# Optimization experiments

Hardware: AMD Instinct MI355X
Metric: run time of the kernel (lower is better)

The kernel has to match this reference:

```python
import jax, jax.numpy as jnp
import numpy as np

# Model dims (match torch defaults)
B, LF, FEAT = 2, 64, 80          # batch, local frames, mel features
H, SKIP, A = 64, 256, 256        # block hidden, skip_size, signal_channels
NL, CYC = 24, 6                  # num_layers, cycle_size
UP_K, UP_REP = 4, 75             # ConvTranspose kernel/stride, frame repeat
S = LF * UP_K * UP_REP           # signal length = 19200


def setup_inputs() -> dict:
    key = jax.random.key(0)
    ks = jax.random.split(key, 16)
    r = lambda i, sh: jax.random.normal(ks[i], sh, jnp.float32) * 0.1
    return {
        'local_features': jax.random.normal(ks[0], (B, LF, FEAT), jnp.float32),
        'gold_signal': jax.random.uniform(ks[1], (B, S), jnp.float32, minval=-1.0, maxval=1.0),
        'embed_w': r(2, (H,)), 'embed_b': r(3, (H,)),
        'tconv_w': r(4, (FEAT, FEAT, UP_K)), 'tconv_b': r(5, (FEAT,)),
        'cond_w': r(6, (NL * 2 * H, FEAT)), 'cond_b': r(7, (NL * 2 * H,)),
        'dilate_w': r(8, (NL, 2 * H, H, 2)), 'dilate_b': r(9, (NL, 2 * H)),
        'res_w': r(10, (NL - 1, H, H)), 'res_b': r(11, (NL - 1, H)),
        'skip_w': r(12, (NL, SKIP, H)), 'skip_b': r(13, (NL, SKIP)),
        'out1_w': r(14, (A, SKIP)), 'out2_w': r(15, (A, A)),
    }


def _causal_dilated(x, w, b, d):
    # x [B,C,T], w [O,C,2]; left-pad by d == torch padding=d then slicing off last d
    y = jax.lax.conv_general_dilated(x, w, window_strides=(1,), padding=[(d, 0)],
                                     rhs_dilation=(d,),
                                     dimension_numbers=('NCH', 'OIH', 'NCH'))
    return y + b[None, :, None]


def reference(local_features, gold_signal, embed_w, embed_b, tconv_w, tconv_b,
              cond_w, cond_b, dilate_w, dilate_b, res_w, res_b,
              skip_w, skip_b, out1_w, out2_w):
    # --- ConditionalFeaturesUpsample ---
    lf = jnp.transpose(local_features, (0, 2, 1))  # [B,FEAT,LF]
    # ConvTranspose1d(kernel=stride=UP_K): out[:, :, UP_K*i+k] = sum_c w[c,:,k]*x[:,c,i]
    up = jnp.einsum('bci,cok->boik', lf, tconv_w).reshape(B, FEAT, LF * UP_K)
    up = up + tconv_b[None, :, None]
    cond = jnp.einsum('oc,bct->bot', cond_w, up) + cond_b[None, :, None]  # [B, NL*2H, LF*4]
    cond = jnp.repeat(cond, UP_REP, axis=-1)                               # [B, NL*2H, S]
    cond = cond.reshape(B, NL, 2 * H, S)
    # --- embed (1x1 conv on 1-channel signal) ---
    x = gold_signal[:, None, :] * embed_w[None, :, None] + embed_b[None, :, None]  # [B,H,S]
    # --- residual stack ---
    skip_acc = jnp.zeros((B, SKIP, S), x.dtype)
    for i in range(NL):
        d = 2 ** (i % CYC)
        y = _causal_dilated(x, dilate_w[i], dilate_b[i], d) + cond[:, i]
        g = jnp.tanh(y[:, :H]) * jax.nn.sigmoid(y[:, H:])
        skip_acc = skip_acc + jnp.einsum('oc,bct->bot', skip_w[i], g) + skip_b[i][None, :, None]
        if i < NL - 1:
            x = jnp.einsum('oc,bct->bot', res_w[i], g) + res_b[i][None, :, None] + x
    # --- output head: ReLU -> 1x1 -> ReLU -> 1x1 -> LogSoftmax(channels) ---
    h = jax.nn.relu(skip_acc)
    h = jax.nn.relu(jnp.einsum('oc,bct->bot', out1_w, h))
    logits = jnp.einsum('oc,bct->bot', out2_w, h)
    return jax.nn.log_softmax(logits, axis=1)  # [B, A, S]
```

## Files before the change

### kernel.cpp

```cpp
#include <hip/hip_runtime.h>
#include <hip/hip_bf16.h>
#include <cstdint>
#include <cstddef>

namespace {

constexpr int kB = 2, kLF = 64, kFEAT = 80, kSKIP = 256, kA = 256;
constexpr int kNL = 24, kT4 = 256;
constexpr int kS = 19200;
constexpr int kGR = 64;
constexpr int kXR = kGR + kS;
constexpr int kK = kNL * 64;
constexpr int kNS = kB * kS;
constexpr int kP2 = 72;

typedef __attribute__((ext_vector_type(8))) short bf8_t;
typedef __attribute__((ext_vector_type(4))) float f4_t;

__device__ inline unsigned short f2bu(float f) {
  __hip_bfloat16 h = __float2bfloat16(f);
  return __builtin_bit_cast(unsigned short, h);
}
__device__ inline float b2f(unsigned short u) {
  unsigned x = (unsigned)u << 16;
  return __builtin_bit_cast(float, x);
}
__device__ inline float fast_gate(float a, float b) {
  a = fminf(fmaxf(a, -30.f), 30.f);
  b = fminf(fmaxf(b, -30.f), 30.f);
  const float ea = __expf(-2.f * a);
  const float eb = __expf(-b);
  return (1.f - ea) * __fdividef(1.f, (1.f + ea) * (1.f + eb));
}

__global__ void prep_kernel(const float* __restrict__ dw, const float* __restrict__ rw,
                            const float* __restrict__ sw, const float* __restrict__ w1,
                            const float* __restrict__ w2, unsigned short* __restrict__ wcb,
                            unsigned short* __restrict__ wrb, unsigned short* __restrict__ swb2,
                            unsigned short* __restrict__ w1f, unsigned short* __restrict__ w2f) {
  int idx = blockIdx.x * 256 + threadIdx.x;
  const int n0 = kNL * 2 * 128 * 64;
  const int n1 = (kNL - 1) * 64 * 64;
  const int n2 = 256 * kK;
  const int n3 = 65536;
  if (idx < n0) {
    int r = idx;
    const int l = r / 16384; r -= l * 16384;
    const int tap = r / 8192; r -= tap * 8192;
    const int o = r / 64; const int h = r - o * 64;
    wcb[idx] = f2bu(dw[((l * 128 + o) * 64 + h) * 2 + tap]);
    return;
  }
  idx -= n0;
  if (idx < n1) { wrb[idx] = f2bu(rw[idx]); return; }
  idx -= n1;
  if (idx < n2) {
    const int q = idx & 31;
    const int rest = idx >> 5;
    const int o = rest & 255;
    const int t = rest >> 8;
    const int kk = t & 1, kb = t >> 1;
    const int h = kk * 32 + q;
    swb2[idx] = f2bu(sw[((size_t)(kb * 256 + o)) * 64 + h]);
    return;
  }
  idx -= n2;
  if (idx < n3) {
    const int q = idx & 31;
    const int rest = idx >> 5;
    const int a = rest & 255, kk = rest >> 8;
    w1f[idx] = f2bu(w1[a * 256 + kk * 32 + q]);
    return;
  }
  idx -= n3;
  if (idx < n3) {
    const int q = idx & 31;
    const int rest = idx >> 5;
    const int a = rest & 255, kk = rest >> 8;
    w2f[idx] = f2bu(w2[a * 256 + kk * 32 + q]);
  }
}

__global__ void up_kernel(const float* __restrict__ lf, const float* __restrict__ tw,
                          const float* __restrict__ tb, float* __restrict__ up) {
  const int t40 = blockIdx.x * 16, b = blockIdx.y;
  __shared__ float lfS[4][80];
  const int tid = threadIdx.x;
  for (int idx = tid; idx < 320; idx += 256) {
    const int rr = idx / 80, cc = idx - rr * 80;
    lfS[rr][cc] = lf[((size_t)b * kLF + (t40 >> 2) + rr) * kFEAT + cc];
  }
  __syncthreads();
  const int t4l = tid & 15;
  const int cq = tid >> 4;
  const int ifr = t4l >> 2, kk = t4l & 3;
  for (int q = 0; q < 5; ++q) {
    const int c = cq * 5 + q;
    float s = tb[c];
    for (int cc = 0; cc < 80; ++cc) s += lfS[ifr][cc] * tw[(cc * 80 + c) * 4 + kk];
    up[((size_t)b * kFEAT + c) * 256 + t40 + t4l] = s;
  }
}

__global__ __launch_bounds__(256) void cond_gemm_kernel(
    const float* __restrict__ up, const float* __restrict__ cw,
    const float* __restrict__ cb, const float* __restrict__ dbf,
    float* __restrict__ cond) {
  const int o0 = blockIdx.x * 128, t40 = blockIdx.y * 64, b = blockIdx.z;
  __shared__ float upS[80][68];
  __shared__ float WS[128][84];
  const int tid = threadIdx.x;
  for (int r = 0; r < 5; ++r) {
    const int f4 = r * 256 + tid;
    const int row = f4 >> 4, c4 = (f4 & 15) << 2;
    *reinterpret_cast<float4*>(&upS[row][c4]) =
        *reinterpret_cast<const float4*>(up + ((size_t)b * kFEAT + row) * 256 + t40 + c4);
  }
  for (int r = 0; r < 10; ++r) {
    const int f4 = r * 256 + tid;
    const int row = f4 / 20, c4 = (f4 % 20) * 4;
    *reinterpret_cast<float4*>(&WS[row][c4]) =
        *reinterpret_cast<const float4*>(cw + (size_t)(o0 + row) * kFEAT + c4);
  }
  __syncthreads();
  const int tx = tid & 15, oy = tid >> 4;
  float4 acc[8];
#pragma unroll
  for (int j = 0; j < 8; ++j) acc[j] = make_float4(0.f, 0.f, 0.f, 0.f);
  for (int k0 = 0; k0 < 80; k0 += 4) {
    float4 b0 = *reinterpret_cast<const float4*>(&upS[k0 + 0][tx * 4]);
    float4 b1 = *reinterpret_cast<const float4*>(&upS[k0 + 1][tx * 4]);
    float4 b2 = *reinterpret_cast<const float4*>(&upS[k0 + 2][tx * 4]);
    float4 b3 = *reinterpret_cast<const float4*>(&upS[k0 + 3][tx * 4]);
#pragma unroll
    for (int j = 0; j < 8; ++j) {
      const float4 wj = *reinterpret_cast<const float4*>(&WS[oy * 8 + j][k0]);
      float4 a = acc[j];
      a.x += wj.x * b0.x + wj.y * b1.x + wj.z * b2.x + wj.w * b3.x;
      a.y += wj.x * b0.y + wj.y * b1.y + wj.z * b2.y + wj.w * b3.y;
      a.z += wj.x * b0.z + wj.y * b1.z + wj.z * b2.z + wj.w * b3.z;
      a.w += wj.x * b0.w + wj.y * b1.w + wj.z * b2.w + wj.w * b3.w;
      acc[j] = a;
    }
  }
  __syncthreads();
  float* ws2 = &WS[0][0];
#pragma unroll
  for (int j = 0; j < 8; ++j) {
    const int ol = oy * 8 + j;
    const int og = o0 + ol;
    const float bias = cb[og] + dbf[og];
    ws2[ol * 69 + tx * 4 + 0] = acc[j].x + bias;
    ws2[ol * 69 + tx * 4 + 1] = acc[j].y + bias;
    ws2[ol * 69 + tx * 4 + 2] = acc[j].z + bias;
    ws2[ol * 69 + tx * 4 + 3] = acc[j].w + bias;
  }
  __syncthreads();
  for (int r = 0; r < 8; ++r) {
    const int f = r * 256 + tid;
    const int row = f >> 5, c4 = (f & 31) << 2;
    float4 v;
    v.x = ws2[(c4 + 0) * 69 + row];
    v.y = ws2[(c4 + 1) * 69 + row];
    v.z = ws2[(c4 + 2) * 69 + row];
    v.w = ws2[(c4 + 3) * 69 + row];
    *reinterpret_cast<float4*>(cond + ((size_t)b * kT4 + t40 + row) * 3072 + o0 + c4) = v;
  }
}

__global__ void bias_sum_kernel(const float* __restrict__ sb, float* __restrict__ bs) {
  const int o = threadIdx.x;
  float s = 0.f;
  for (int i = 0; i < kNL; ++i) s += sb[i * kSKIP + o];
  bs[o] = s;
}

__global__ void embed_kernel(const float* __restrict__ sig, const float* __restrict__ ew,
                             const float* __restrict__ eb, unsigned short* __restrict__ xA,
                             unsigned short* __restrict__ xB) {
  const int idx = blockIdx.x * 256 + threadIdx.x;
  if (idx >= kB * kXR * 8) return;
  const int c8 = (idx & 7) << 3;
  const int row = (idx >> 3) % kXR;
  const int b = idx / (kXR * 8);
  const size_t off = ((size_t)b * kXR + row) * 64 + c8;
  if (row < kGR) {
    uint4 z = {0u, 0u, 0u, 0u};
    *reinterpret_cast<uint4*>(xA + off) = z;
    *reinterpret_cast<uint4*>(xB + off) = z;
  } else {
    const float s = sig[b * kS + row - kGR];
    unsigned short v[8];
#pragma unroll
    for (int q = 0; q < 8; ++q) v[q] = f2bu(s * ew[c8 + q] + eb[c8 + q]);
    *reinterpret_cast<uint4*>(xA + off) = *reinterpret_cast<uint4*>(v);
  }
}

__global__ __launch_bounds__(256) void layer_kernel(
    const unsigned short* __restrict__ x_in, unsigned short* __restrict__ x_out,
    const unsigned short* __restrict__ wcb,
    const unsigned short* __restrict__ wrb,
    const float* __restrict__ cond, const float* __restrict__ rb,
    unsigned short* __restrict__ gbuf, int layer, int d, int write_x) {
  const int b = blockIdx.y;
  const int t0 = blockIdx.x * 64;
  const int tid = threadIdx.x;
  const int lane = tid & 63, wv = tid >> 6;
  const int l15 = lane & 15, l4 = lane >> 4;
  const int nw = wv * 16;

  __shared__ alignas(16) unsigned short Wc[2][128][kP2];
  __shared__ alignas(16) unsigned short Wr[64][kP2];
  __shared__ alignas(16) unsigned short xww[96][kP2];
  __shared__ alignas(16) unsigned short gt[64][kP2];
  __shared__ alignas(16) unsigned short xo[64][kP2];
  __shared__ float cnd[2][128];
  __shared__ float rbs[64];

  const int c0 = t0 / 75;
  {
    const int ci = tid >> 7, o = tid & 127;
    int cc = c0 + ci; if (cc > 255) cc = 255;
    cnd[ci][o] = cond[((size_t)b * kT4 + cc) * 3072 + layer * 128 + o];
  }
  if (tid < 64) rbs[tid] = write_x ? rb[tid] : 0.f;
  for (int r = 0; r < 8; ++r) {
    const int f = r * 256 + tid;
    const int row = f >> 3, c8 = (f & 7) << 3;
    *reinterpret_cast<uint4*>(&Wc[row >> 7][row & 127][c8]) =
        *reinterpret_cast<const uint4*>(wcb + row * 64 + c8);
  }
  if (write_x) {
    for (int r = 0; r < 2; ++r) {
      const int f = r * 256 + tid;
      const int row = f >> 3, c8 = (f & 7) << 3;
      *reinterpret_cast<uint4*>(&Wr[row][c8]) =
          *reinterpret_cast<const uint4*>(wrb + row * 64 + c8);
    }
  }
  const unsigned short* xwin = x_in + ((size_t)b * kXR + kGR + t0 - 32) * 64;
  for (int r = 0; r < 3; ++r) {
    const int f = r * 256 + tid;
    const int row = f >> 3, c8 = (f & 7) << 3;
    *reinterpret_cast<uint4*>(&xww[row][c8]) =
        *reinterpret_cast<const uint4*>(xwin + (size_t)row * 64 + c8);
  }
  __syncthreads();

  f4_t acc[8];
#pragma unroll
  for (int i = 0; i < 8; ++i) acc[i] = (f4_t){0.f, 0.f, 0.f, 0.f};
#pragma unroll
  for (int kk = 0; kk < 2; ++kk) {
    const int ko = kk * 32 + l4 * 8;
    const bf8_t b1 = *reinterpret_cast<const bf8_t*>(&xww[32 + nw + l15][ko]);
    const bf8_t b0 = *reinterpret_cast<const bf8_t*>(&xww[32 - d + nw + l15][ko]);
#pragma unroll
    for (int mi = 0; mi < 8; ++mi) {
      const bf8_t a1 = *reinterpret_cast<const bf8_t*>(&Wc[1][mi * 16 + l15][ko]);
      acc[mi] = __builtin_amdgcn_mfma_f32_16x16x32_bf16(a1, b1, acc[mi], 0, 0, 0);
      const bf8_t a0 = *reinterpret_cast<const bf8_t*>(&Wc[0][mi * 16 + l15][ko]);
      acc[mi] = __builtin_amdgcn_mfma_f32_16x16x32_bf16(a0, b0, acc[mi], 0, 0, 0);
    }
  }

  const int t_lane = t0 + nw + l15;
  const int ci = (t_lane >= (c0 + 1) * 75) ? 1 : 0;
#pragma unroll
  for (int mi = 0; mi < 4; ++mi) {
    float gg[4];
#pragma unroll
    for (int r = 0; r < 4; ++r) {
      const int olo = mi * 16 + l4 * 4 + r;
      gg[r] = fast_gate(acc[mi][r] + cnd[ci][olo], acc[mi + 4][r] + cnd[ci][olo + 64]);
    }
    const int hb = mi * 16 + l4 * 4;
    *reinterpret_cast<unsigned int*>(&gt[nw + l15][hb]) =
        (unsigned)f2bu(gg[0]) | ((unsigned)f2bu(gg[1]) << 16);
    *reinterpret_cast<unsigned int*>(&gt[nw + l15][hb + 2]) =
        (unsigned)f2bu(gg[2]) | ((unsigned)f2bu(gg[3]) << 16);
  }

  {
    unsigned short* gb = gbuf + ((size_t)layer * kNS + b * kS + t0) * 64;
#pragma unroll
    for (int r = 0; r < 2; ++r) {
      const int q = lane * 2 + r;
      const int row = nw + (q >> 3);
      const int c = q & 7;
      const int cs = c ^ (row & 7);
      *reinterpret_cast<uint4*>(gb + (size_t)row * 64 + (cs << 3)) =
          *reinterpret_cast<const uint4*>(&gt[row][c << 3]);
    }
  }

  if (write_x) {
    f4_t accr[4];
#pragma unroll
    for (int i = 0; i < 4; ++i) accr[i] = (f4_t){0.f, 0.f, 0.f, 0.f};
#pragma unroll
    for (int kk = 0; kk < 2; ++kk) {
      const int ko = kk * 32 + l4 * 8;
      const bf8_t bfr = *reinterpret_cast<const bf8_t*>(&gt[nw + l15][ko]);
#pragma unroll
      for (int mi = 0; mi < 4; ++mi) {
        const bf8_t afr = *reinterpret_cast<const bf8_t*>(&Wr[mi * 16 + l15][ko]);
        accr[mi] = __builtin_amdgcn_mfma_f32_16x16x32_bf16(afr, bfr, accr[mi], 0, 0, 0);
      }
    }
#pragma unroll
    for (int mi = 0; mi < 4; ++mi) {
      const int h0 = mi * 16 + l4 * 4;
      const unsigned u01 = *reinterpret_cast<const unsigned*>(&xww[32 + nw + l15][h0]);
      const unsigned u23 = *reinterpret_cast<const unsigned*>(&xww[32 + nw + l15][h0 + 2]);
      const float x0 = accr[mi][0] + rbs[h0 + 0] + b2f((unsigned short)(u01 & 0xffffu));
      const float x1 = accr[mi][1] + rbs[h0 + 1] + b2f((unsigned short)(u01 >> 16));
      const float x2 = accr[mi][2] + rbs[h0 + 2] + b2f((unsigned short)(u23 & 0xffffu));
      const float x3 = accr[mi][3] + rbs[h0 + 3] + b2f((unsigned short)(u23 >> 16));
      *reinterpret_cast<unsigned*>(&xo[nw + l15][h0]) =
          (unsigned)f2bu(x0) | ((unsigned)f2bu(x1) << 16);
      *reinterpret_cast<unsigned*>(&xo[nw + l15][h0 + 2]) =
          (unsigned)f2bu(x2) | ((unsigned)f2bu(x3) << 16);
    }
    unsigned short* xob = x_out + ((size_t)b * kXR + kGR + t0) * 64;
#pragma unroll
    for (int r = 0; r < 2; ++r) {
      const int q = lane * 2 + r;
      const int row = nw + (q >> 3), c8 = (q & 7) << 3;
      *reinterpret_cast<uint4*>(xob + (size_t)row * 64 + c8) =
          *reinterpret_cast<const uint4*>(&xo[row][c8]);
    }
  }
}

__global__ __launch_bounds__(512) void skip_kernel(
    const unsigned short* __restrict__ gbuf, const unsigned short* __restrict__ swb2,
    const float* __restrict__ bs, unsigned short* __restrict__ skipb) {
  const int n0 = blockIdx.x * 64;
  __shared__ alignas(16) unsigned short Ag[2][128][64];
  const int tid = threadIdx.x, lane = tid & 63, wv = tid >> 6;
  const int l15 = lane & 15, l4 = lane >> 4;
  const int ow = wv * 32;
  f4_t acc[4][2];
#pragma unroll
  for (int i = 0; i < 4; ++i)
#pragma unroll
    for (int j = 0; j < 2; ++j) acc[i][j] = (f4_t){0.f, 0.f, 0.f, 0.f};

#define STAGE2(kb2, buf)                                                               \
  {                                                                                    \
    const unsigned short* s0 =                                                         \
        gbuf + ((size_t)((kb2)*2) * kNS + n0) * 64 + (size_t)tid * 8;                  \
    const unsigned short* s1 =                                                         \
        gbuf + ((size_t)((kb2)*2 + 1) * kNS + n0) * 64 + (size_t)tid * 8;              \
    __builtin_amdgcn_global_load_lds(                                                  \
        (const __attribute__((address_space(1))) unsigned int*)s0,                     \
        (__attribute__((address_space(3))) unsigned int*)(&Ag[buf][wv * 8][0]),        \
        16, 0, 0);                                                                     \
    __builtin_amdgcn_global_load_lds(                                                  \
        (const __attribute__((address_space(1))) unsigned int*)s1,                     \
        (__attribute__((address_space(3))) unsigned int*)(&Ag[buf][64 + wv * 8][0]),   \
        16, 0, 0);                                                                     \
  }

  STAGE2(0, 0);
  for (int kb2 = 0; kb2 < 12; ++kb2) {
    __syncthreads();
    if (kb2 < 11) STAGE2(kb2 + 1, (kb2 + 1) & 1);
    const int bi = kb2 & 1;
#pragma unroll
    for (int sub = 0; sub < 2; ++sub) {
      const int kb = kb2 * 2 + sub;
#pragma unroll
      for (int kk = 0; kk < 2; ++kk) {
        bf8_t afr[4], bfr[2];
#pragma unroll
        for (int i = 0; i < 4; ++i) {
          const int row = i * 16 + l15;
          const int slot = (kk * 4 + l4) ^ (row & 7);
          afr[i] = *reinterpret_cast<const bf8_t*>(&Ag[bi][sub * 64 + row][slot << 3]);
        }
#pragma unroll
        for (int j = 0; j < 2; ++j)
          bfr[j] = *reinterpret_cast<const bf8_t*>(
              swb2 + ((size_t)(kb * 2 + kk) * 256 + ow + j * 16 + l15) * 32 + l4 * 8);
#pragma unroll
        for (int mi = 0; mi < 4; ++mi)
#pragma unroll
          for (int ni = 0; ni < 2; ++ni)
            acc[mi][ni] = __builtin_amdgcn_mfma_f32_16x16x32_bf16(afr[mi], bfr[ni],
                                                                  acc[mi][ni], 0, 0, 0);
      }
    }
  }
#undef STAGE2
#pragma unroll
  for (int mi = 0; mi < 4; ++mi)
#pragma unroll
    for (int ni = 0; ni < 2; ++ni) {
      const int o = ow + ni * 16 + l15;
      const float bo = bs[o];
#pragma unroll
      for (int r = 0; r < 4; ++r) {
        const int n = n0 + mi * 16 + l4 * 4 + r;
        skipb[(size_t)n * 256 + o] = f2bu(acc[mi][ni][r] + bo);
      }
    }
}

__device__ inline unsigned int relu2(unsigned int u) {
  const unsigned lo = (u & 0x8000u) ? 0u : (u & 0xFFFFu);
  const unsigned hi = (u & 0x80000000u) ? 0u : (u & 0xFFFF0000u);
  return lo | hi;
}

__global__ __launch_bounds__(256) void head_kernel(
    const unsigned short* __restrict__ skipb, const unsigned short* __restrict__ w1f,
    const unsigned short* __restrict__ w2f, float* __restrict__ out) {
  const int b = blockIdx.y;
  const int t0 = blockIdx.x * 32;
  const int n0 = b * kS + t0;
  __shared__ __align__(16) char smem[16896 * 2];
  __shared__ float lsa[32];
  unsigned short (*A1)[264] = reinterpret_cast<unsigned short(*)[264]>(smem);
  unsigned short (*H1)[264] = reinterpret_cast<unsigned short(*)[264]>(smem + 16896);
  float (*LG)[260] = reinterpret_cast<float(*)[260]>(smem);

  const int tid = threadIdx.x, lane = tid & 63, wv = tid >> 6;
  const int l15 = lane & 15, l4 = lane >> 4;
  for (int r = 0; r < 4; ++r) {
    const int ch = r * 256 + tid;
    const int row = ch >> 5, c8 = (ch & 31) << 3;
    uint4 v = *reinterpret_cast<const uint4*>(skipb + (size_t)(n0 + row) * 256 + c8);
    v.x = relu2(v.x); v.y = relu2(v.y); v.z = relu2(v.z); v.w = relu2(v.w);
    *reinterpret_cast<uint4*>(&A1[row][c8]) = v;
  }
  __syncthreads();
  f4_t a1[2][4];
#pragma unroll
  for (int i = 0; i < 2; ++i)
#pragma unroll
    for (int j = 0; j < 4; ++j) a1[i][j] = (f4_t){0.f, 0.f, 0.f, 0.f};
  for (int kk = 0; kk < 8; ++kk) {
    const int ko = kk * 32 + l4 * 8;
    bf8_t afr[2], bfr[4];
#pragma unroll
    for (int i = 0; i < 2; ++i)
      afr[i] = *reinterpret_cast<const bf8_t*>(&A1[i * 16 + l15][ko]);
#pragma unroll
    for (int j = 0; j < 4; ++j)
      bfr[j] = *reinterpret_cast<const bf8_t*>(
          w1f + ((size_t)kk * 256 + wv * 64 + j * 16 + l15) * 32 + l4 * 8);
#pragma unroll
    for (int mi = 0; mi < 2; ++mi)
#pragma unroll
      for (int ni = 0; ni < 4; ++ni)
        a1[mi][ni] = __builtin_amdgcn_mfma_f32_16x16x32_bf16(afr[mi], bfr[ni],
                                                             a1[mi][ni], 0, 0, 0);
  }
#pragma unroll
  for (int mi = 0; mi < 2; ++mi)
#pragma unroll
    for (int ni = 0; ni < 4; ++ni)
#pragma unroll
      for (int r = 0; r < 4; ++r)
        H1[mi * 16 + l4 * 4 + r][wv * 64 + ni * 16 + l15] =
            f2bu(fmaxf(a1[mi][ni][r], 0.f));
  __syncthreads();
  f4_t a2[2][4];
#pragma unroll
  for (int i = 0; i < 2; ++i)
#pragma unroll
    for (int j = 0; j < 4; ++j) a2[i][j] = (f4_t){0.f, 0.f, 0.f, 0.f};
  for (int kk = 0; kk < 8; ++kk) {
    const int ko = kk * 32 + l4 * 8;
    bf8_t afr[2], bfr[4];
#pragma unroll
    for (int i = 0; i < 2; ++i)
      afr[i] = *reinterpret_cast<const bf8_t*>(&H1[i * 16 + l15][ko]);
#pragma unroll
    for (int j = 0; j < 4; ++j)
      bfr[j] = *reinterpret_cast<const bf8_t*>(
          w2f + ((size_t)kk * 256 + wv * 64 + j * 16 + l15) * 32 + l4 * 8);
#pragma unroll
    for (int mi = 0; mi < 2; ++mi)
#pragma unroll
      for (int ni = 0; ni < 4; ++ni)
        a2[mi][ni] = __builtin_amdgcn_mfma_f32_16x16x32_bf16(afr[mi], bfr[ni],
                                                             a2[mi][ni], 0, 0, 0);
  }
  __syncthreads();
#pragma unroll
  for (int mi = 0; mi < 2; ++mi)
#pragma unroll
    for (int ni = 0; ni < 4; ++ni)
#pragma unroll
      for (int r = 0; r < 4; ++r)
        LG[mi * 16 + l4 * 4 + r][wv * 64 + ni * 16 + l15] = a2[mi][ni][r];
  __syncthreads();
  const int rn = tid >> 3, s = tid & 7;
  float m = -3.4e38f;
  for (int a = s; a < 256; a += 8) m = fmaxf(m, LG[rn][a]);
  m = fmaxf(m, __shfl_xor(m, 1));
  m = fmaxf(m, __shfl_xor(m, 2));
  m = fmaxf(m, __shfl_xor(m, 4));
  float sum = 0.f;
  for (int a = s; a < 256; a += 8) sum += __expf(LG[rn][a] - m);
  sum += __shfl_xor(sum, 1);
  sum += __shfl_xor(sum, 2);
  sum += __shfl_xor(sum, 4);
  if (s == 0) lsa[rn] = m + __logf(sum);
  __syncthreads();
  float* ob = out + (size_t)b * kA * kS + t0;
  for (int q = 0; q < 8; ++q) {
    const int a = q * 32 + (tid >> 3);
    const int t4 = (tid & 7) * 4;
    float4 v;
    v.x = LG[t4 + 0][a] - lsa[t4 + 0];
    v.y = LG[t4 + 1][a] - lsa[t4 + 1];
    v.z = LG[t4 + 2][a] - lsa[t4 + 2];
    v.w = LG[t4 + 3][a] - lsa[t4 + 3];
    *reinterpret_cast<float4*>(ob + (size_t)a * kS + t4) = v;
  }
}

}

extern "C" void kernel_launch(void* const* d_in, const int* in_sizes, int n_in,
                              void* d_out, int out_size, void* d_ws, size_t ws_size,
                              hipStream_t stream) {
  const float* lf  = (const float*)d_in[0];
  const float* sig = (const float*)d_in[1];
  const float* ew  = (const float*)d_in[2];
  const float* eb  = (const float*)d_in[3];
  const float* tw  = (const float*)d_in[4];
  const float* tb  = (const float*)d_in[5];
  const float* cw  = (const float*)d_in[6];
  const float* cb  = (const float*)d_in[7];
  const float* dw  = (const float*)d_in[8];
  const float* dbf = (const float*)d_in[9];
  const float* rw  = (const float*)d_in[10];
  const float* rb  = (const float*)d_in[11];
  const float* sw  = (const float*)d_in[12];
  const float* sb  = (const float*)d_in[13];
  const float* w1  = (const float*)d_in[14];
  const float* w2  = (const float*)d_in[15];
  float* out = (float*)d_out;

  char* p = (char*)d_ws;
  float* cond = (float*)p;            p += (size_t)kB * kT4 * 3072 * 4;
  unsigned short* xA = (unsigned short*)p;    p += (size_t)kB * kXR * 64 * 2;
  unsigned short* xB = (unsigned short*)p;    p += (size_t)kB * kXR * 64 * 2;
  unsigned short* gbuf = (unsigned short*)p;  p += (size_t)kNL * kNS * 64 * 2;
  unsigned short* skipb = (unsigned short*)p; p += (size_t)kNS * 256 * 2;
  unsigned short* wcb = (unsigned short*)p;   p += (size_t)kNL * 2 * 128 * 64 * 2;
  unsigned short* wrb = (unsigned short*)p;   p += (size_t)(kNL - 1) * 64 * 64 * 2;
  unsigned short* swb2 = (unsigned short*)p;  p += (size_t)256 * kK * 2;
  unsigned short* w1f = (unsigned short*)p;   p += (size_t)256 * 256 * 2;
  unsigned short* w2f = (unsigned short*)p;   p += (size_t)256 * 256 * 2;
  float* bs = (float*)p;              p += 1024;
  float* upb = (float*)p;             p += (size_t)kB * kFEAT * 256 * 4;

  prep_kernel<<<(1011712 + 255) / 256, 256, 0, stream>>>(dw, rw, sw, w1, w2,
                                                         wcb, wrb, swb2, w1f, w2f);
  up_kernel<<<dim3(16, 2), 256, 0, stream>>>(lf, tw, tb, upb);
  cond_gemm_kernel<<<dim3(24, 4, 2), 256, 0, stream>>>(upb, cw, cb, dbf, cond);
  bias_sum_kernel<<<1, 256, 0, stream>>>(sb, bs);
  embed_kernel<<<(kB * kXR * 8 + 255) / 256, 256, 0, stream>>>(sig, ew, eb, xA, xB);

  unsigned short* xcur = xA;
  unsigned short* xnxt = xB;
  for (int l = 0; l < kNL; ++l) {
    const int d = 1 << (l % 6);
    const int wx = (l < kNL - 1) ? 1 : 0;
    layer_kernel<<<dim3(300, 2), 256, 0, stream>>>(
        xcur, xnxt, wcb + (size_t)l * 16384, wrb + (size_t)(wx ? l : 0) * 4096,
        cond, rb + (size_t)(wx ? l : 0) * 64, gbuf, l, d, wx);
    if (wx) { unsigned short* tmp = xcur; xcur = xnxt; xnxt = tmp; }
  }
  skip_kernel<<<600, 512, 0, stream>>>(gbuf, swb2, bs, skipb);
  head_kernel<<<dim3(600, 2), 256, 0, stream>>>(skipb, w1f, w2f, out);
}
```

Baseline: 412.1 us.

## Read layer weights directly from global in MFMA fragment layout; fold upsample into cond GEMM

The dilated-conv and residual weights are repacked at prep time into an MFMA-fragment-friendly layout, so layer_kernel loads A fragments straight from global/L2 instead of staging them through shared memory. This drops the per-block weight copy and shrinks shared memory use per block, which may raise occupancy, at the cost of repeated global loads inside the MFMA loop. Separately, the transposed-conv upsample is algebraically folded into the conditioning weights (W2 = tconv_w x cond_w, plus a precomputed bias). The cond GEMM therefore works directly on the local features, and up_kernel is replaced by extra prep kernels.

```diff
diff --git a/kernel.cpp b/kernel.cpp
--- a/kernel.cpp
+++ b/kernel.cpp
@@ -35,24 +35,37 @@
 
 __global__ void prep_kernel(const float* __restrict__ dw, const float* __restrict__ rw,
                             const float* __restrict__ sw, const float* __restrict__ w1,
-                            const float* __restrict__ w2, unsigned short* __restrict__ wcb,
-                            unsigned short* __restrict__ wrb, unsigned short* __restrict__ swb2,
-                            unsigned short* __restrict__ w1f, unsigned short* __restrict__ w2f) {
+                            const float* __restrict__ w2, const float* __restrict__ cw,
+                            unsigned short* __restrict__ wcf, unsigned short* __restrict__ wrf,
+                            unsigned short* __restrict__ swb2, unsigned short* __restrict__ w1f,
+                            unsigned short* __restrict__ w2f, float* __restrict__ cwT) {
   int idx = blockIdx.x * 256 + threadIdx.x;
   const int n0 = kNL * 2 * 128 * 64;
   const int n1 = (kNL - 1) * 64 * 64;
   const int n2 = 256 * kK;
   const int n3 = 65536;
+  const int n4 = 80 * 3072;
   if (idx < n0) {
-    int r = idx;
-    const int l = r / 16384; r -= l * 16384;
-    const int tap = r / 8192; r -= tap * 8192;
-    const int o = r / 64; const int h = r - o * 64;
-    wcb[idx] = f2bu(dw[((l * 128 + o) * 64 + h) * 2 + tap]);
+    const int l = idx / 16384, r = idx % 16384;
+    const int q = r & 31;
+    const int rest = r >> 5;
+    const int o = rest & 127;
+    const int tk = rest >> 7;
+    const int tap = tk >> 1, kk = tk & 1;
+    const int h = kk * 32 + q;
+    wcf[idx] = f2bu(dw[((l * 128 + o) * 64 + h) * 2 + tap]);
     return;
   }
   idx -= n0;
-  if (idx < n1) { wrb[idx] = f2bu(rw[idx]); return; }
+  if (idx < n1) {
+    const int l = idx / 4096, r = idx % 4096;
+    const int q = r & 31;
+    const int rest = r >> 5;
+    const int o = rest & 63;
+    const int kk = rest >> 6;
+    wrf[idx] = f2bu(rw[(l * 64 + o) * 64 + kk * 32 + q]);
+    return;
+  }
   idx -= n1;
   if (idx < n2) {
     const int q = idx & 31;
@@ -60,8 +73,7 @@
     const int o = rest & 255;
     const int t = rest >> 8;
     const int kk = t & 1, kb = t >> 1;
-    const int h = kk * 32 + q;
-    swb2[idx] = f2bu(sw[((size_t)(kb * 256 + o)) * 64 + h]);
+    swb2[idx] = f2bu(sw[((size_t)(kb * 256 + o)) * 64 + kk * 32 + q]);
     return;
   }
   idx -= n2;
@@ -78,93 +90,87 @@
     const int rest = idx >> 5;
     const int a = rest & 255, kk = rest >> 8;
     w2f[idx] = f2bu(w2[a * 256 + kk * 32 + q]);
-  }
-}
-
-__global__ void up_kernel(const float* __restrict__ lf, const float* __restrict__ tw,
-                          const float* __restrict__ tb, float* __restrict__ up) {
-  const int t40 = blockIdx.x * 16, b = blockIdx.y;
-  __shared__ float lfS[4][80];
-  const int tid = threadIdx.x;
-  for (int idx = tid; idx < 320; idx += 256) {
-    const int rr = idx / 80, cc = idx - rr * 80;
-    lfS[rr][cc] = lf[((size_t)b * kLF + (t40 >> 2) + rr) * kFEAT + cc];
-  }
-  __syncthreads();
-  const int t4l = tid & 15;
-  const int cq = tid >> 4;
-  const int ifr = t4l >> 2, kk = t4l & 3;
-  for (int q = 0; q < 5; ++q) {
-    const int c = cq * 5 + q;
-    float s = tb[c];
-    for (int cc = 0; cc < 80; ++cc) s += lfS[ifr][cc] * tw[(cc * 80 + c) * 4 + kk];
-    up[((size_t)b * kFEAT + c) * 256 + t40 + t4l] = s;
-  }
+    return;
+  }
+  idx -= n3;
+  if (idx < n4) {
+    const int c = idx / 3072, o = idx % 3072;
+    cwT[idx] = cw[o * 80 + c];
+  }
+}
+
+__global__ __launch_bounds__(256) void prep_w2_kernel(const float* __restrict__ tw,
+                                                      const float* __restrict__ cwT,
+                                                      float* __restrict__ W2) {
+  const int o = blockIdx.x * 256 + threadIdx.x;
+  const int kk = blockIdx.y;
+  __shared__ float twS[80][80];
+  for (int i = threadIdx.x; i < 6400; i += 256) twS[i / 80][i % 80] = tw[i * 4 + kk];
+  __syncthreads();
+  float cwrow[80];
+#pragma unroll
+  for (int c = 0; c < 80; ++c) cwrow[c] = cwT[c * 3072 + o];
+  for (int cc = 0; cc < 80; ++cc) {
+    float acc = 0.f;
+#pragma unroll
+    for (int c = 0; c < 80; ++c) acc += twS[cc][c] * cwrow[c];
+    W2[((size_t)(kk * 80 + cc)) * 3072 + o] = acc;
+  }
+}
+
+__global__ void bias2_kernel(const float* __restrict__ cwT, const float* __restrict__ tb,
+                             const float* __restrict__ cb, const float* __restrict__ dbf,
+                             float* __restrict__ bias2) {
+  const int o = blockIdx.x * 256 + threadIdx.x;
+  float acc = cb[o] + dbf[o];
+  for (int c = 0; c < 80; ++c) acc += cwT[c * 3072 + o] * tb[c];
+  bias2[o] = acc;
 }
 
 __global__ __launch_bounds__(256) void cond_gemm_kernel(
-    const float* __restrict__ up, const float* __restrict__ cw,
-    const float* __restrict__ cb, const float* __restrict__ dbf,
-    float* __restrict__ cond) {
-  const int o0 = blockIdx.x * 128, t40 = blockIdx.y * 64, b = blockIdx.z;
-  __shared__ float upS[80][68];
-  __shared__ float WS[128][84];
+    const float* __restrict__ lf, const float* __restrict__ W2,
+    const float* __restrict__ bias2, float* __restrict__ cond) {
+  const int o0 = blockIdx.x * 64;
+  const int kk = blockIdx.y;
+  const int b = blockIdx.z;
+  __shared__ float lfS[64][84];
+  __shared__ float WS[80][68];
   const int tid = threadIdx.x;
   for (int r = 0; r < 5; ++r) {
     const int f4 = r * 256 + tid;
+    const int row = f4 / 20, c4 = (f4 % 20) * 4;
+    *reinterpret_cast<float4*>(&lfS[row][c4]) =
+        *reinterpret_cast<const float4*>(lf + ((size_t)b * kLF + row) * kFEAT + c4);
+  }
+  for (int r = 0; r < 5; ++r) {
+    const int f4 = r * 256 + tid;
     const int row = f4 >> 4, c4 = (f4 & 15) << 2;
-    *reinterpret_cast<float4*>(&upS[row][c4]) =
-        *reinterpret_cast<const float4*>(up + ((size_t)b * kFEAT + row) * 256 + t40 + c4);
-  }
-  for (int r = 0; r < 10; ++r) {
-    const int f4 = r * 256 + tid;
-    const int row = f4 / 20, c4 = (f4 % 20) * 4;
     *reinterpret_cast<float4*>(&WS[row][c4]) =
-        *reinterpret_cast<const float4*>(cw + (size_t)(o0 + row) * kFEAT + c4);
+        *reinterpret_cast<const float4*>(W2 + ((size_t)(kk * 80 + row)) * 3072 + o0 + c4);
   }
   __syncthreads();
   const int tx = tid & 15, oy = tid >> 4;
-  float4 acc[8];
-#pragma unroll
-  for (int j = 0; j < 8; ++j) acc[j] = make_float4(0.f, 0.f, 0.f, 0.f);
-  for (int k0 = 0; k0 < 80; k0 += 4) {
-    float4 b0 = *reinterpret_cast<const float4*>(&upS[k0 + 0][tx * 4]);
-    float4 b1 = *reinterpret_cast<const float4*>(&upS[k0 + 1][tx * 4]);
-    float4 b2 = *reinterpret_cast<const float4*>(&upS[k0 + 2][tx * 4]);
-    float4 b3 = *reinterpret_cast<const float4*>(&upS[k0 + 3][tx * 4]);
-#pragma unroll
-    for (int j = 0; j < 8; ++j) {
-      const float4 wj = *reinterpret_cast<const float4*>(&WS[oy * 8 + j][k0]);
-      float4 a = acc[j];
-      a.x += wj.x * b0.x + wj.y * b1.x + wj.z * b2.x + wj.w * b3.x;
-      a.y += wj.x * b0.y + wj.y * b1.y + wj.z * b2.y + wj.w * b3.y;
-      a.z += wj.x * b0.z + wj.y * b1.z + wj.z * b2.z + wj.w * b3.z;
-      a.w += wj.x * b0.w + wj.y * b1.w + wj.z * b2.w + wj.w * b3.w;
-      acc[j] = a;
-    }
-  }
-  __syncthreads();
-  float* ws2 = &WS[0][0];
-#pragma unroll
-  for (int j = 0; j < 8; ++j) {
-    const int ol = oy * 8 + j;
-    const int og = o0 + ol;
-    const float bias = cb[og] + dbf[og];
-    ws2[ol * 69 + tx * 4 + 0] = acc[j].x + bias;
-    ws2[ol * 69 + tx * 4 + 1] = acc[j].y + bias;
-    ws2[ol * 69 + tx * 4 + 2] = acc[j].z + bias;
-    ws2[ol * 69 + tx * 4 + 3] = acc[j].w + bias;
-  }
-  __syncthreads();
-  for (int r = 0; r < 8; ++r) {
-    const int f = r * 256 + tid;
-    const int row = f >> 5, c4 = (f & 31) << 2;
-    float4 v;
-    v.x = ws2[(c4 + 0) * 69 + row];
-    v.y = ws2[(c4 + 1) * 69 + row];
-    v.z = ws2[(c4 + 2) * 69 + row];
-    v.w = ws2[(c4 + 3) * 69 + row];
-    *reinterpret_cast<float4*>(cond + ((size_t)b * kT4 + t40 + row) * 3072 + o0 + c4) = v;
+  float acc[4][4];
+#pragma unroll
+  for (int j = 0; j < 4; ++j)
+#pragma unroll
+    for (int r = 0; r < 4; ++r) acc[j][r] = 0.f;
+  for (int c = 0; c < 80; ++c) {
+    const float4 w = *reinterpret_cast<const float4*>(&WS[c][oy * 4]);
+#pragma unroll
+    for (int j = 0; j < 4; ++j) {
+      const float a = lfS[tx * 4 + j][c];
+      acc[j][0] += a * w.x; acc[j][1] += a * w.y;
+      acc[j][2] += a * w.z; acc[j][3] += a * w.w;
+    }
+  }
+  const float4 bb = *reinterpret_cast<const float4*>(bias2 + o0 + oy * 4);
+#pragma unroll
+  for (int j = 0; j < 4; ++j) {
+    const int t4 = (tx * 4 + j) * 4 + kk;
+    float4 v = make_float4(acc[j][0] + bb.x, acc[j][1] + bb.y,
+                           acc[j][2] + bb.z, acc[j][3] + bb.w);
+    *reinterpret_cast<float4*>(cond + ((size_t)b * kT4 + t4) * 3072 + o0 + oy * 4) = v;
   }
 }
 
@@ -199,8 +205,8 @@
 
 __global__ __launch_bounds__(256) void layer_kernel(
     const unsigned short* __restrict__ x_in, unsigned short* __restrict__ x_out,
-    const unsigned short* __restrict__ wcb,
-    const unsigned short* __restrict__ wrb,
+    const unsigned short* __restrict__ wcf,
+    const unsigned short* __restrict__ wrf,
     const float* __restrict__ cond, const float* __restrict__ rb,
     unsigned short* __restrict__ gbuf, int layer, int d, int write_x) {
   const int b = blockIdx.y;
@@ -210,8 +216,6 @@
   const int l15 = lane & 15, l4 = lane >> 4;
   const int nw = wv * 16;
 
-  __shared__ alignas(16) unsigned short Wc[2][128][kP2];
-  __shared__ alignas(16) unsigned short Wr[64][kP2];
   __shared__ alignas(16) unsigned short xww[96][kP2];
   __shared__ alignas(16) unsigned short gt[64][kP2];
   __shared__ alignas(16) unsigned short xo[64][kP2];
@@ -225,20 +229,6 @@
     cnd[ci][o] = cond[((size_t)b * kT4 + cc) * 3072 + layer * 128 + o];
   }
   if (tid < 64) rbs[tid] = write_x ? rb[tid] : 0.f;
-  for (int r = 0; r < 8; ++r) {
-    const int f = r * 256 + tid;
-    const int row = f >> 3, c8 = (f & 7) << 3;
-    *reinterpret_cast<uint4*>(&Wc[row >> 7][row & 127][c8]) =
-        *reinterpret_cast<const uint4*>(wcb + row * 64 + c8);
-  }
-  if (write_x) {
-    for (int r = 0; r < 2; ++r) {
-      const int f = r * 256 + tid;
-      const int row = f >> 3, c8 = (f & 7) << 3;
-      *reinterpret_cast<uint4*>(&Wr[row][c8]) =
-          *reinterpret_cast<const uint4*>(wrb + row * 64 + c8);
-    }
-  }
   const unsigned short* xwin = x_in + ((size_t)b * kXR + kGR + t0 - 32) * 64;
   for (int r = 0; r < 3; ++r) {
     const int f = r * 256 + tid;
@@ -258,9 +248,11 @@
     const bf8_t b0 = *reinterpret_cast<const bf8_t*>(&xww[32 - d + nw + l15][ko]);
 #pragma unroll
     for (int mi = 0; mi < 8; ++mi) {
-      const bf8_t a1 = *reinterpret_cast<const bf8_t*>(&Wc[1][mi * 16 + l15][ko]);
+      const bf8_t a1 = *reinterpret_cast<const bf8_t*>(
+          wcf + ((size_t)(2 + kk) * 128 + mi * 16 + l15) * 32 + l4 * 8);
       acc[mi] = __builtin_amdgcn_mfma_f32_16x16x32_bf16(a1, b1, acc[mi], 0, 0, 0);
-      const bf8_t a0 = *reinterpret_cast<const bf8_t*>(&Wc[0][mi * 16 + l15][ko]);
+      const bf8_t a0 = *reinterpret_cast<const bf8_t*>(
+          wcf + ((size_t)(0 + kk) * 128 + mi * 16 + l15) * 32 + l4 * 8);
       acc[mi] = __builtin_amdgcn_mfma_f32_16x16x32_bf16(a0, b0, acc[mi], 0, 0, 0);
     }
   }
@@ -305,7 +297,8 @@
       const bf8_t bfr = *reinterpret_cast<const bf8_t*>(&gt[nw + l15][ko]);
 #pragma unroll
       for (int mi = 0; mi < 4; ++mi) {
-        const bf8_t afr = *reinterpret_cast<const bf8_t*>(&Wr[mi * 16 + l15][ko]);
+        const bf8_t afr = *reinterpret_cast<const bf8_t*>(
+            wrf + ((size_t)kk * 64 + mi * 16 + l15) * 32 + l4 * 8);
         accr[mi] = __builtin_amdgcn_mfma_f32_16x16x32_bf16(afr, bfr, accr[mi], 0, 0, 0);
       }
     }
@@ -554,18 +547,22 @@
   unsigned short* xB = (unsigned short*)p;    p += (size_t)kB * kXR * 64 * 2;
   unsigned short* gbuf = (unsigned short*)p;  p += (size_t)kNL * kNS * 64 * 2;
   unsigned short* skipb = (unsigned short*)p; p += (size_t)kNS * 256 * 2;
-  unsigned short* wcb = (unsigned short*)p;   p += (size_t)kNL * 2 * 128 * 64 * 2;
-  unsigned short* wrb = (unsigned short*)p;   p += (size_t)(kNL - 1) * 64 * 64 * 2;
+  unsigned short* wcf = (unsigned short*)p;   p += (size_t)kNL * 2 * 128 * 64 * 2;
+  unsigned short* wrf = (unsigned short*)p;   p += (size_t)(kNL - 1) * 64 * 64 * 2;
   unsigned short* swb2 = (unsigned short*)p;  p += (size_t)256 * kK * 2;
   unsigned short* w1f = (unsigned short*)p;   p += (size_t)256 * 256 * 2;
   unsigned short* w2f = (unsigned short*)p;   p += (size_t)256 * 256 * 2;
   float* bs = (float*)p;              p += 1024;
-  float* upb = (float*)p;             p += (size_t)kB * kFEAT * 256 * 4;
-
-  prep_kernel<<<(1011712 + 255) / 256, 256, 0, stream>>>(dw, rw, sw, w1, w2,
-                                                         wcb, wrb, swb2, w1f, w2f);
-  up_kernel<<<dim3(16, 2), 256, 0, stream>>>(lf, tw, tb, upb);
-  cond_gemm_kernel<<<dim3(24, 4, 2), 256, 0, stream>>>(upb, cw, cb, dbf, cond);
+  float* cwT = (float*)p;             p += (size_t)80 * 3072 * 4;
+  float* W2 = (float*)p;              p += (size_t)4 * 80 * 3072 * 4;
+  float* bias2 = (float*)p;           p += (size_t)3072 * 4;
+
+  const int prep_n = 393216 + 94208 + 393216 + 65536 + 65536 + 245760;
+  prep_kernel<<<(prep_n + 255) / 256, 256, 0, stream>>>(dw, rw, sw, w1, w2, cw,
+                                                        wcf, wrf, swb2, w1f, w2f, cwT);
+  prep_w2_kernel<<<dim3(12, 4), 256, 0, stream>>>(tw, cwT, W2);
+  bias2_kernel<<<12, 256, 0, stream>>>(cwT, tb, cb, dbf, bias2);
+  cond_gemm_kernel<<<dim3(48, 4, 2), 256, 0, stream>>>(lf, W2, bias2, cond);
   bias_sum_kernel<<<1, 256, 0, stream>>>(sb, bs);
   embed_kernel<<<(kB * kXR * 8 + 255) / 256, 256, 0, stream>>>(sig, ew, eb, xA, xB);
 
@@ -575,7 +572,7 @@
     const int d = 1 << (l % 6);
     const int wx = (l < kNL - 1) ? 1 : 0;
     layer_kernel<<<dim3(300, 2), 256, 0, stream>>>(
-        xcur, xnxt, wcb + (size_t)l * 16384, wrb + (size_t)(wx ? l : 0) * 4096,
+        xcur, xnxt, wcf + (size_t)l * 16384, wrf + (size_t)(wx ? l : 0) * 4096,
         cond, rb + (size_t)(wx ? l : 0) * 64, gbuf, l, d, wx);
     if (wx) { unsigned short* tmp = xcur; xcur = xnxt; xnxt = tmp; }
   }
```

After: 457.6 us. 1.11x slower.
